# Optimization experiments

Hardware: AMD Instinct MI355X
Metric: run time of the kernel (lower is better)

## Reference

```python
import jax, jax.numpy as jnp
import numpy as np

# Model constants (from Equilibrium3BConfig + hardcoded MambaBlock args)
D_MODEL = 2560
D_INNER = 5120          # expand=2
N_STATE = 128           # d_state
HEADS = 80              # d_inner // headdim
P_HEAD = 64             # headdim
D_CONV = 4
CONV_DIM = D_INNER + 2 * N_STATE        # 5376 (x, B, C share the conv)
D_IN_PROJ = 2 * D_INNER + 2 * N_STATE + HEADS  # 10576 (z, xBC, dt)
N_EXPERTS = 16
TOP_K = 2
M_INTER = 864
MS_INTER = 1728
EPS = 1e-6


def _rms(x, w, eps=EPS):
    xf = x.astype(jnp.float32)
    xf = xf * jax.lax.rsqrt(jnp.mean(xf * xf, axis=-1, keepdims=True) + eps)
    return w * xf.astype(x.dtype)


def setup_inputs() -> dict:
    key = jax.random.key(0)
    ks = jax.random.split(key, 16)
    b, l = 1, 1024
    s = 0.02  # weight scale, keeps activations sane through the deep block
    return {
        "hidden_states": jax.random.normal(ks[0], (b, l, D_MODEL), jnp.float32),
        "w_in": jax.random.normal(ks[1], (D_MODEL, D_IN_PROJ), jnp.float32) * s,
        "conv_w": jax.random.normal(ks[2], (CONV_DIM, D_CONV), jnp.float32) * s,
        "conv_b": jnp.zeros((CONV_DIM,), jnp.float32),
        "dt_bias": jax.random.normal(ks[3], (HEADS,), jnp.float32) * s,
        "A_log": jax.random.normal(ks[4], (HEADS,), jnp.float32) * s,
        "D": jnp.ones((HEADS,), jnp.float32),
        "mamba_norm_w": jnp.ones((D_INNER,), jnp.float32),
        "w_out": jax.random.normal(ks[5], (D_INNER, D_MODEL), jnp.float32) * s,
        "ln1_w": jnp.ones((D_MODEL,), jnp.float32),
        "ln2_w": jnp.ones((D_MODEL,), jnp.float32),
        "router_w": jax.random.normal(ks[6], (D_MODEL, N_EXPERTS), jnp.float32) * s,
        "we_gate": jax.random.normal(ks[7], (N_EXPERTS, D_MODEL, M_INTER), jnp.float32) * s,
        "we_up": jax.random.normal(ks[8], (N_EXPERTS, D_MODEL, M_INTER), jnp.float32) * s,
        "we_down": jax.random.normal(ks[9], (N_EXPERTS, M_INTER, D_MODEL), jnp.float32) * s,
        "ws_gate": jax.random.normal(ks[10], (D_MODEL, MS_INTER), jnp.float32) * s,
        "ws_up": jax.random.normal(ks[11], (D_MODEL, MS_INTER), jnp.float32) * s,
        "ws_down": jax.random.normal(ks[12], (MS_INTER, D_MODEL), jnp.float32) * s,
    }


def _forward(hidden_states, w_in, conv_w, conv_b, dt_bias, A_log, D, mamba_norm_w,
             w_out, ln1_w, ln2_w, router_w, we_gate, we_up, we_down,
             ws_gate, ws_up, ws_down):
    b, l, d = hidden_states.shape

    # ---- Mamba2 (selective scan) sub-block ----
    residual = hidden_states
    x = _rms(hidden_states, ln1_w)
    zxbcdt = x @ w_in  # [b, l, 10576]
    z, xBC, dt = jnp.split(zxbcdt, [D_INNER, D_INNER + CONV_DIM], axis=-1)

    # depthwise causal conv over (x, B, C) channels, then SiLU
    xBC_t = xBC.transpose(0, 2, 1)  # [b, c, l]
    conv = jax.lax.conv_general_dilated(
        xBC_t, conv_w[:, None, :], (1,), [(D_CONV - 1, 0)],
        feature_group_count=CONV_DIM, dimension_numbers=("NCH", "OIH", "NCH"))
    xBC = jax.nn.silu((conv + conv_b[None, :, None]).transpose(0, 2, 1))
    xs, Bc, Cc = jnp.split(xBC, [D_INNER, D_INNER + N_STATE], axis=-1)

    dt = jax.nn.softplus(dt + dt_bias)          # [b, l, h]
    A = -jnp.exp(A_log)                          # [h]
    xh = xs.reshape(b, l, HEADS, P_HEAD)

    # time-major for scan
    dt_l = dt.transpose(1, 0, 2)                 # [l, b, h]
    xh_l = xh.transpose(1, 0, 2, 3)              # [l, b, h, p]
    B_l = Bc.transpose(1, 0, 2)                  # [l, b, n]
    C_l = Cc.transpose(1, 0, 2)                  # [l, b, n]

    def step(h, inp):
        dt_t, x_t, B_t, C_t = inp
        dA = jnp.exp(dt_t * A)                   # [b, h]
        h = h * dA[..., None, None] + (dt_t[..., None] * x_t)[..., None] * B_t[:, None, None, :]
        y = jnp.einsum("bhpn,bn->bhp", h, C_t)
        return h, y

    h0 = jnp.zeros((b, HEADS, P_HEAD, N_STATE), hidden_states.dtype)
    _, y_l = jax.lax.scan(step, h0, (dt_l, xh_l, B_l, C_l))
    y_l = y_l + D[None, None, :, None] * xh_l    # skip term
    y = y_l.transpose(1, 0, 2, 3).reshape(b, l, D_INNER)
    y = _rms(y * jax.nn.silu(z), mamba_norm_w)   # gated RMSNorm
    hidden = residual + y @ w_out

    # ---- DeepSeekMoE sub-block ----
    residual2 = hidden
    xm = _rms(hidden, ln2_w).reshape(b * l, d)
    logits = xm @ router_w
    probs = jax.nn.softmax(logits.astype(jnp.float32), axis=-1)
    topv, topi = jax.lax.top_k(probs, TOP_K)
    topv = topv / jnp.sum(topv, axis=-1, keepdims=True)  # renormalize top-k
    wdense = jnp.sum(jax.nn.one_hot(topi, N_EXPERTS, dtype=xm.dtype)
                     * topv[..., None].astype(xm.dtype), axis=1)  # [T, E]

    # routed experts (SwiGLU), dense-masked faithful math
    hexp = (jax.nn.silu(jnp.einsum("td,edm->tem", xm, we_gate))
            * jnp.einsum("td,edm->tem", xm, we_up))
    y_routed = jnp.einsum("tem,emd,te->td", hexp, we_down, wdense)

    # shared experts (single fused SwiGLU MLP)
    y_shared = (jax.nn.silu(xm @ ws_gate) * (xm @ ws_up)) @ ws_down

    moe = (y_routed + y_shared).reshape(b, l, d)
    return residual2 + moe


def reference(hidden_states, w_in, conv_w, conv_b, dt_bias, A_log, D, mamba_norm_w,
              w_out, ln1_w, ln2_w, router_w, we_gate, we_up, we_down,
              ws_gate, ws_up, ws_down):
    return _forward(hidden_states, w_in, conv_w, conv_b, dt_bias, A_log, D,
                    mamba_norm_w, w_out, ln1_w, ln2_w, router_w,
                    we_gate, we_up, we_down, ws_gate, ws_up, ws_down)
```

## Files before the change

### kernel.cpp

```cpp
#include <hip/hip_runtime.h>

typedef __attribute__((ext_vector_type(4))) float f32x4;
typedef __attribute__((ext_vector_type(8))) __bf16 bf16x8;
typedef __attribute__((ext_vector_type(4))) __bf16 bf16x4;
typedef __attribute__((ext_vector_type(8))) _Float16 f16x8;
typedef __attribute__((ext_vector_type(4))) _Float16 f16x4;

#define D_MODEL 2560
#define D_INNER 5120
#define N_STATE 128
#define HEADS 80
#define P_HEAD 64
#define CONV_DIM 5376
#define D_INPROJ 10576
#define SEQ 1024
#define NCHUNK 32
#define QCHUNK 32
#define NEXP 16
#define M_INTER 864
#define MS_INTER 1728
#define NSLOT 2048
#define NSLOTP 2176

__device__ __forceinline__ float siluf(float x) { return x / (1.f + __expf(-x)); }

__device__ __forceinline__ int swz_p(int k4, int P) {
  return (k4 & ~31) | ((((k4 >> 3) & 3) ^ P) << 3) | (k4 & 7);
}
__device__ __forceinline__ int swz64(int k4, int row) {
  return (k4 & ~63) | (((((k4 >> 3) & 7) ^ (row & 7)) << 3)) | (k4 & 7);
}

__device__ __forceinline__ void gl16(const __bf16* g, __bf16* l) {
  __builtin_amdgcn_global_load_lds((const __attribute__((address_space(1))) unsigned int*)g,
                                   (__attribute__((address_space(3))) unsigned int*)l, 16, 0, 0);
}

__device__ __forceinline__ float block_sum256(float v, float* red) {
#pragma unroll
  for (int m = 32; m > 0; m >>= 1) v += __shfl_xor(v, m, 64);
  int w = threadIdx.x >> 6;
  if ((threadIdx.x & 63) == 0) red[w] = v;
  __syncthreads();
  return red[0] + red[1] + red[2] + red[3];
}

template <bool FP16>
__global__ __launch_bounds__(256) void k_rmsnorm_p(const float* __restrict__ in,
                                                   const float* __restrict__ w,
                                                   float* __restrict__ f32out,
                                                   __bf16* __restrict__ ph,
                                                   __bf16* __restrict__ pdh,
                                                   __bf16* __restrict__ pdl, int D) {
  __shared__ float red[4];
  int t = blockIdx.x, tid = threadIdx.x;
  const float* x = in + (size_t)t * D;
  int nd4 = D >> 2;
  float ss = 0.f;
  for (int i = tid; i < nd4; i += 256) {
    float4 v = ((const float4*)x)[i];
    ss += v.x * v.x + v.y * v.y + v.z * v.z + v.w * v.w;
  }
  float tot = block_sum256(ss, red);
  float r = rsqrtf(tot / (float)D + 1e-6f);
  int P = (t >> 1) & 3;
  for (int i = tid; i < nd4; i += 256) {
    float4 v = ((const float4*)x)[i];
    float4 wv = ((const float4*)w)[i];
    float4 o;
    o.x = wv.x * v.x * r; o.y = wv.y * v.y * r; o.z = wv.z * v.z * r; o.w = wv.w * v.w * r;
    if (f32out) ((float4*)(f32out + (size_t)t * D))[i] = o;
    int p64 = swz64(i * 4, t);
    if constexpr (FP16) {
      f16x4 hv;
      hv[0] = (_Float16)o.x; hv[1] = (_Float16)o.y; hv[2] = (_Float16)o.z; hv[3] = (_Float16)o.w;
      *(f16x4*)&ph[(size_t)t * D + p64] = hv;
    } else {
      bf16x4 hv;
      hv[0] = (__bf16)o.x; hv[1] = (__bf16)o.y; hv[2] = (__bf16)o.z; hv[3] = (__bf16)o.w;
      *(bf16x4*)&ph[(size_t)t * D + p64] = hv;
    }
    if (pdh) {
      int p = swz_p(i * 4, P);
      bf16x4 hv, lv;
      hv[0] = (__bf16)o.x; hv[1] = (__bf16)o.y; hv[2] = (__bf16)o.z; hv[3] = (__bf16)o.w;
      lv[0] = (__bf16)(o.x - (float)hv[0]); lv[1] = (__bf16)(o.y - (float)hv[1]);
      lv[2] = (__bf16)(o.z - (float)hv[2]); lv[3] = (__bf16)(o.w - (float)hv[3]);
      *(bf16x4*)&pdh[(size_t)t * D + p] = hv;
      *(bf16x4*)&pdl[(size_t)t * D + p] = lv;
    }
  }
}

template <bool SPLIT, bool FP16>
__global__ __launch_bounds__(256) void k_transW(const float* __restrict__ W, int ld, int K, int N,
                                                __bf16* __restrict__ Th, __bf16* __restrict__ Tl) {
  __shared__ float T[64][65];
  const int n0 = blockIdx.x * 64, k0 = blockIdx.y * 64, tid = threadIdx.x;
#pragma unroll
  for (int i = 0; i < 16; i++) {
    int idx = tid + i * 256;
    int k = idx >> 6, n = idx & 63;
    float v = 0.f;
    if (n0 + n < N) v = W[(size_t)(k0 + k) * ld + n0 + n];
    T[k][n] = v;
  }
  __syncthreads();
#pragma unroll
  for (int i = 0; i < 4; i++) {
    int idx = tid + i * 256;
    int n = idx >> 4, p4 = (idx & 15) * 4;
    int nn = n0 + n;
    if constexpr (SPLIT) {
      int P = (nn >> 1) & 3;
      bf16x4 hv, lv;
#pragma unroll
      for (int e = 0; e < 4; e++) {
        int p = p4 + e;
        int kk = (p & ~31) | ((((p >> 3) & 3) ^ P) << 3) | (p & 7);
        float v = T[kk][n];
        __bf16 h = (__bf16)v;
        hv[e] = h;
        lv[e] = (__bf16)(v - (float)h);
      }
      *(bf16x4*)&Th[(size_t)nn * K + k0 + p4] = hv;
      *(bf16x4*)&Tl[(size_t)nn * K + k0 + p4] = lv;
    } else if constexpr (FP16) {
      f16x4 hv;
#pragma unroll
      for (int e = 0; e < 4; e++) {
        int p = p4 + e;
        int kk = swz64(p, nn);
        hv[e] = (_Float16)T[kk][n];
      }
      *(f16x4*)&Th[(size_t)nn * K + k0 + p4] = hv;
    } else {
      bf16x4 hv;
#pragma unroll
      for (int e = 0; e < 4; e++) {
        int p = p4 + e;
        int kk = swz64(p, nn);
        hv[e] = (__bf16)T[kk][n];
      }
      *(bf16x4*)&Th[(size_t)nn * K + k0 + p4] = hv;
    }
  }
}

template <bool SPLIT, bool FP16, int BK, bool PIPE>
__global__ __launch_bounds__(256) void k_gemm2(const __bf16* __restrict__ Ah,
                                               const __bf16* __restrict__ Al,
                                               const __bf16* __restrict__ Bh,
                                               const __bf16* __restrict__ Bl,
                                               float* __restrict__ C,
                                               int M, int N, int K, int ks, int nst) {
  constexpr int PLE = 128 * BK;
  constexpr int NPL = SPLIT ? 4 : 2;
  constexpr int NBUF = PIPE ? 2 : 1;
  constexpr int CALLS = PLE / 2048;
  constexpr int CPR = BK / 8;
  constexpr int RPC = 256 / CPR;
  constexpr int KSUB = BK / 32;
  __shared__ __bf16 lds[NBUF * NPL * PLE];

  const int tid = threadIdx.x;
  const int T = gridDim.x * gridDim.y * gridDim.z;
  const int linear = blockIdx.x + gridDim.x * (blockIdx.y + gridDim.y * blockIdx.z);
  const int s_idx = (linear & 7) * (T >> 3) + (linear >> 3);
  const int bm = s_idx & 7;
  const int g = s_idx >> 3;
  const int bn = g % gridDim.y;
  const int z = g / gridDim.y;

  const int m0 = bm * 128, n0 = bn * 128;
  const int s0 = (int)(((long long)z * nst) / ks);
  const int s1 = (int)(((long long)(z + 1) * nst) / ks);
  float* __restrict__ Cp = C + (size_t)z * M * N;

  const int lane = tid & 63, wid = tid >> 6;
  const int wr = wid >> 1, wc = wid & 1;
  const int l16 = lane & 15, kl = lane >> 4;

  const int srow = tid / CPR;
  const int schunk = (tid % CPR) * 8;
  size_t aB[CALLS], bB[CALLS];
#pragma unroll
  for (int i = 0; i < CALLS; i++) {
    aB[i] = (size_t)(m0 + srow + RPC * i) * K + schunk;
    bB[i] = (size_t)(n0 + srow + RPC * i) * K + schunk;
  }

  int aoff[4][KSUB], boff[4][KSUB];
#pragma unroll
  for (int mi = 0; mi < 4; mi++) {
    int ra = wr * 64 + mi * 16 + l16;
    int rb = wc * 64 + mi * 16 + l16;
#pragma unroll
    for (int kk = 0; kk < KSUB; kk++) {
      if constexpr (BK == 32) {
        aoff[mi][kk] = ra * 64 + ((kl ^ ((ra >> 1) & 3)) << 4);
        boff[mi][kk] = rb * 64 + ((kl ^ ((rb >> 1) & 3)) << 4);
      } else {
        aoff[mi][kk] = ra * (2 * BK) + (((kk * 4 + kl) ^ (ra & 7)) << 4);
        boff[mi][kk] = rb * (2 * BK) + (((kk * 4 + kl) ^ (rb & 7)) << 4);
      }
    }
  }

  f32x4 acc[4][4];
#pragma unroll
  for (int mi = 0; mi < 4; mi++)
#pragma unroll
    for (int ni = 0; ni < 4; ni++) acc[mi][ni] = f32x4{0.f, 0.f, 0.f, 0.f};

  auto STAGE = [&](int b, int kof) {
    __bf16* L = lds + (size_t)b * NPL * PLE;
#pragma unroll
    for (int i = 0; i < CALLS; i++) {
      gl16(Ah + aB[i] + kof, L + (tid + i * 256) * 8);
      gl16(Bh + bB[i] + kof, L + (SPLIT ? 2 : 1) * PLE + (tid + i * 256) * 8);
      if constexpr (SPLIT) {
        gl16(Al + aB[i] + kof, L + PLE + (tid + i * 256) * 8);
        gl16(Bl + bB[i] + kof, L + 3 * PLE + (tid + i * 256) * 8);
      }
    }
  };

  auto COMPUTE = [&](const __bf16* L) {
    const char* AsH = (const char*)L;
    const char* BsH = (const char*)(L + (SPLIT ? 2 : 1) * PLE);
#pragma unroll
    for (int kk = 0; kk < KSUB; kk++) {
      if constexpr (!SPLIT && FP16) {
        f16x8 ah[4], bh[4];
#pragma unroll
        for (int mi = 0; mi < 4; mi++) ah[mi] = *(const f16x8*)(AsH + aoff[mi][kk]);
#pragma unroll
        for (int ni = 0; ni < 4; ni++) bh[ni] = *(const f16x8*)(BsH + boff[ni][kk]);
#pragma unroll
        for (int mi = 0; mi < 4; mi++)
#pragma unroll
          for (int ni = 0; ni < 4; ni++)
            acc[mi][ni] = __builtin_amdgcn_mfma_f32_16x16x32_f16(ah[mi], bh[ni], acc[mi][ni], 0, 0, 0);
      } else {
        bf16x8 ah[4], bh[4];
#pragma unroll
        for (int mi = 0; mi < 4; mi++) ah[mi] = *(const bf16x8*)(AsH + aoff[mi][kk]);
#pragma unroll
        for (int ni = 0; ni < 4; ni++) bh[ni] = *(const bf16x8*)(BsH + boff[ni][kk]);
#pragma unroll
        for (int mi = 0; mi < 4; mi++)
#pragma unroll
          for (int ni = 0; ni < 4; ni++)
            acc[mi][ni] = __builtin_amdgcn_mfma_f32_16x16x32_bf16(ah[mi], bh[ni], acc[mi][ni], 0, 0, 0);
        if constexpr (SPLIT) {
          const char* AsL = (const char*)(L + PLE);
          const char* BsL = (const char*)(L + 3 * PLE);
          bf16x8 al[4], bl[4];
#pragma unroll
          for (int mi = 0; mi < 4; mi++) al[mi] = *(const bf16x8*)(AsL + aoff[mi][kk]);
#pragma unroll
          for (int ni = 0; ni < 4; ni++) bl[ni] = *(const bf16x8*)(BsL + boff[ni][kk]);
#pragma unroll
          for (int mi = 0; mi < 4; mi++)
#pragma unroll
            for (int ni = 0; ni < 4; ni++) {
              acc[mi][ni] = __builtin_amdgcn_mfma_f32_16x16x32_bf16(ah[mi], bl[ni], acc[mi][ni], 0, 0, 0);
              acc[mi][ni] = __builtin_amdgcn_mfma_f32_16x16x32_bf16(al[mi], bh[ni], acc[mi][ni], 0, 0, 0);
            }
        }
      }
    }
  };

  if constexpr (PIPE) {
    STAGE(0, s0 * BK);
    __syncthreads();
    int cur = 0;
    for (int s = s0; s < s1; ++s) {
      if (s + 1 < s1) STAGE(cur ^ 1, (s + 1) * BK);
      COMPUTE(lds + (size_t)cur * NPL * PLE);
      __syncthreads();
      cur ^= 1;
    }
  } else {
    for (int s = s0; s < s1; ++s) {
      __syncthreads();
      STAGE(0, s * BK);
      __syncthreads();
      COMPUTE(lds);
    }
  }

#pragma unroll
  for (int mi = 0; mi < 4; mi++)
#pragma unroll
    for (int ni = 0; ni < 4; ni++)
#pragma unroll
      for (int r = 0; r < 4; r++) {
        int row = m0 + wr * 64 + mi * 16 + kl * 4 + r;
        int col = n0 + wc * 64 + ni * 16 + l16;
        if (col < N) Cp[(size_t)row * N + col] = acc[mi][ni][r];
      }
}

template <bool RES>
__global__ void k_reduce(const float* __restrict__ Pp, int np, int n4,
                         const float* __restrict__ res, float* __restrict__ out) {
  int i = blockIdx.x * 256 + threadIdx.x;
  int stride = gridDim.x * 256;
  for (; i < n4; i += stride) {
    float4 a = ((const float4*)Pp)[i];
    for (int z = 1; z < np; z++) {
      float4 b = ((const float4*)Pp)[(size_t)z * n4 + i];
      a.x += b.x; a.y += b.y; a.z += b.z; a.w += b.w;
    }
    if constexpr (RES) {
      float4 r0 = ((const float4*)res)[i];
      a.x += r0.x; a.y += r0.y; a.z += r0.z; a.w += r0.w;
    }
    ((float4*)out)[i] = a;
  }
}

__global__ void k_dtfin(const float* __restrict__ dtP, const float* __restrict__ dt_bias,
                        const float* __restrict__ A_log, float* __restrict__ dtp,
                        float* __restrict__ dtA) {
  int t = blockIdx.x, h = threadIdx.x;
  if (h < HEADS) {
    float v = dt_bias[h];
#pragma unroll
    for (int z = 0; z < 8; z++) v += dtP[((size_t)z * SEQ + t) * 80 + h];
    float sp = fmaxf(v, 0.f) + log1pf(expf(-fabsf(v)));
    dtp[t * HEADS + h] = sp;
    dtA[t * HEADS + h] = sp * (-expf(A_log[h]));
  }
}

__global__ __launch_bounds__(256) void k_gatherA(const float* __restrict__ xm,
                                                 const int* __restrict__ perm,
                                                 __bf16* __restrict__ Aslots) {
  int s = blockIdx.x, tid = threadIdx.x;
  int t = perm[s];
  int P = (s >> 1) & 3;
  const float* src = xm + (size_t)t * D_MODEL;
  __bf16* dst = Aslots + (size_t)s * D_MODEL;
  for (int i = tid; i < D_MODEL / 4; i += 256) {
    float4 v = ((const float4*)src)[i];
    int p = swz_p(i * 4, P);
    bf16x4 h;
    h[0] = (__bf16)v.x; h[1] = (__bf16)v.y; h[2] = (__bf16)v.z; h[3] = (__bf16)v.w;
    *(bf16x4*)&dst[p] = h;
  }
}

template <int KS>
__global__ __launch_bounds__(256) void k_gemmE2(const __bf16* __restrict__ Aall,
                                                const float* __restrict__ Bg,
                                                float* __restrict__ Cp,
                                                const int* __restrict__ expOff,
                                                const int* __restrict__ expCnt,
                                                int N, int K, long long strideB) {
  __shared__ __bf16 Asl[2][128 * 32];
  __shared__ __bf16 Bsl[2][128][40];
  const int tid = threadIdx.x;
  const int bn = blockIdx.x, ks = blockIdx.y, e = blockIdx.z;
  const int cnt = expCnt[e], base = expOff[e];
  if (cnt == 0) return;
  const float* Bp = Bg + (long long)e * strideB;
  const int n0 = bn * 128;
  const int kChunk = K / KS, kBeg = ks * kChunk, nIter = kChunk / 32;
  float* __restrict__ Cpl = Cp + (size_t)ks * NSLOTP * N;
  const int lane = tid & 63, wid = tid >> 6;
  const int wr = wid >> 1, wc = wid & 1;
  const int l16 = lane & 15, kl = lane >> 4;
  const int kb = tid >> 5, cb = tid & 31;
  const int arow = tid >> 2, achk = (tid & 3) * 8;
  const bool bok = (n0 + cb * 4) < N;

  int boffs[4];
#pragma unroll
  for (int ni = 0; ni < 4; ni++) boffs[ni] = (wc * 64 + ni * 16 + l16) * 40 + kl * 8;

  for (int bm = 0; bm * 128 < cnt; ++bm) {
    const int rbase = base + bm * 128;
    int aoff[4];
#pragma unroll
    for (int mi = 0; mi < 4; mi++) {
      int r = wr * 64 + mi * 16 + l16;
      int P = ((rbase + r) >> 1) & 3;
      aoff[mi] = r * 64 + ((kl ^ P) << 4);
    }
    f32x4 acc[4][4];
#pragma unroll
    for (int mi = 0; mi < 4; mi++)
#pragma unroll
      for (int ni = 0; ni < 4; ni++) acc[mi][ni] = f32x4{0.f, 0.f, 0.f, 0.f};

    const size_t aBase = (size_t)(rbase + arow) * K + achk + kBeg;
    const size_t aBase2 = aBase + (size_t)64 * K;

    gl16(Aall + aBase, &Asl[0][tid * 8]);
    gl16(Aall + aBase2, &Asl[0][(tid + 256) * 8]);
    {
      const float* src = Bp + (size_t)(kBeg + kb * 4) * N + n0 + cb * 4;
      f32x4 bv[4];
#pragma unroll
      for (int j = 0; j < 4; j++)
        bv[j] = bok ? *(const f32x4*)(src + (size_t)j * N) : f32x4{0.f, 0.f, 0.f, 0.f};
#pragma unroll
      for (int e4 = 0; e4 < 4; e4++) {
        bf16x4 h;
        h[0] = (__bf16)bv[0][e4]; h[1] = (__bf16)bv[1][e4];
        h[2] = (__bf16)bv[2][e4]; h[3] = (__bf16)bv[3][e4];
        *(bf16x4*)&Bsl[0][cb * 4 + e4][kb * 4] = h;
      }
    }
    __syncthreads();
    int cur = 0;
    for (int kt = 0; kt < nIter; ++kt) {
      const bool more = (kt + 1 < nIter);
      f32x4 nv[4];
      if (more) {
        const int kOff = (kt + 1) * 32;
        gl16(Aall + aBase + kOff, &Asl[cur ^ 1][tid * 8]);
        gl16(Aall + aBase2 + kOff, &Asl[cur ^ 1][(tid + 256) * 8]);
        const float* src = Bp + (size_t)(kBeg + kOff + kb * 4) * N + n0 + cb * 4;
#pragma unroll
        for (int j = 0; j < 4; j++)
          nv[j] = bok ? *(const f32x4*)(src + (size_t)j * N) : f32x4{0.f, 0.f, 0.f, 0.f};
      }
      bf16x8 ah[4], bh[4];
#pragma unroll
      for (int mi = 0; mi < 4; mi++) ah[mi] = *(const bf16x8*)((const char*)&Asl[cur][0] + aoff[mi]);
#pragma unroll
      for (int ni = 0; ni < 4; ni++) bh[ni] = *(const bf16x8*)&Bsl[cur][0][boffs[ni]];
#pragma unroll
      for (int mi = 0; mi < 4; mi++)
#pragma unroll
        for (int ni = 0; ni < 4; ni++)
          acc[mi][ni] = __builtin_amdgcn_mfma_f32_16x16x32_bf16(ah[mi], bh[ni], acc[mi][ni], 0, 0, 0);
      if (more) {
#pragma unroll
        for (int e4 = 0; e4 < 4; e4++) {
          bf16x4 h;
          h[0] = (__bf16)nv[0][e4]; h[1] = (__bf16)nv[1][e4];
          h[2] = (__bf16)nv[2][e4]; h[3] = (__bf16)nv[3][e4];
          *(bf16x4*)&Bsl[cur ^ 1][cb * 4 + e4][kb * 4] = h;
        }
      }
      __syncthreads();
      cur ^= 1;
    }
#pragma unroll
    for (int mi = 0; mi < 4; mi++)
#pragma unroll
      for (int ni = 0; ni < 4; ni++)
#pragma unroll
        for (int r = 0; r < 4; r++) {
          int rl = bm * 128 + wr * 64 + mi * 16 + kl * 4 + r;
          int col = n0 + wc * 64 + ni * 16 + l16;
          if (rl < cnt && col < N) Cpl[(size_t)(base + rl) * N + col] = acc[mi][ni][r];
        }
  }
}

__global__ __launch_bounds__(256) void k_silumulE(const float* __restrict__ gP,
                                                  const float* __restrict__ uP,
                                                  const float* __restrict__ slotw,
                                                  __bf16* __restrict__ outp) {
  int s = blockIdx.x, tid = threadIdx.x;
  float w = slotw[s];
  int P = (s >> 1) & 3;
  const size_t PL = (size_t)NSLOTP * M_INTER;
  for (int i = tid; i < M_INTER / 4; i += 256) {
    f32x4 g = f32x4{0.f, 0.f, 0.f, 0.f}, u = f32x4{0.f, 0.f, 0.f, 0.f};
#pragma unroll
    for (int z = 0; z < 4; z++) {
      g += *(const f32x4*)&gP[z * PL + (size_t)s * M_INTER + i * 4];
      u += *(const f32x4*)&uP[z * PL + (size_t)s * M_INTER + i * 4];
    }
    int p = swz_p(i * 4, P);
    bf16x4 h;
    h[0] = (__bf16)(siluf(g[0]) * u[0] * w);
    h[1] = (__bf16)(siluf(g[1]) * u[1] * w);
    h[2] = (__bf16)(siluf(g[2]) * u[2] * w);
    h[3] = (__bf16)(siluf(g[3]) * u[3] * w);
    *(bf16x4*)&outp[(size_t)s * M_INTER + p] = h;
  }
}

__global__ __launch_bounds__(256) void k_silumul_sh2(const float* __restrict__ P4,
                                                     __bf16* __restrict__ outp) {
  int t = blockIdx.x, tid = threadIdx.x;
  const size_t PL = (size_t)SEQ * 3456;
  for (int i = tid; i < MS_INTER / 4; i += 256) {
    f32x4 g = f32x4{0.f, 0.f, 0.f, 0.f}, u = f32x4{0.f, 0.f, 0.f, 0.f};
#pragma unroll
    for (int z = 0; z < 4; z++) {
      g += *(const f32x4*)&P4[z * PL + (size_t)t * 3456 + i * 4];
      u += *(const f32x4*)&P4[z * PL + (size_t)t * 3456 + 1728 + i * 4];
    }
    int p = swz64(i * 4, t);
    bf16x4 h;
    h[0] = (__bf16)(siluf(g[0]) * u[0]);
    h[1] = (__bf16)(siluf(g[1]) * u[1]);
    h[2] = (__bf16)(siluf(g[2]) * u[2]);
    h[3] = (__bf16)(siluf(g[3]) * u[3]);
    *(bf16x4*)&outp[(size_t)t * MS_INTER + p] = h;
  }
}

__global__ void k_conv(const float* __restrict__ zx, const float* __restrict__ cw,
                       const float* __restrict__ cb, float* __restrict__ xBC) {
  int cidx = blockIdx.x * 256 + threadIdx.x;
  int t = blockIdx.y;
  if (cidx < CONV_DIM) {
    float acc = cb[cidx];
#pragma unroll
    for (int j = 0; j < 4; j++) {
      int tt = t - 3 + j;
      if (tt >= 0) acc += zx[(size_t)tt * D_INPROJ + D_INNER + cidx] * cw[cidx * 4 + j];
    }
    xBC[(size_t)t * CONV_DIM + cidx] = siluf(acc);
  }
}

__global__ __launch_bounds__(256) void k_scan_intra(
    const float* __restrict__ xBC, const float* __restrict__ dtp,
    const float* __restrict__ dtA, float* __restrict__ y, float* __restrict__ S,
    float* __restrict__ cumA, float* __restrict__ Atot) {
  __shared__ float Bs[32][128];
  __shared__ float Cs[32][128];
  __shared__ float Xs[32][68];
  __shared__ float Gs[32][33];
  __shared__ float da_s[32], a_s[32], dt_sh[32], w_sh[32];
  int c = blockIdx.x, h = blockIdx.y, tid = threadIdx.x;
  int t0 = c * QCHUNK;
#pragma unroll
  for (int i = 0; i < 4; i++) {
    int id = tid + 256 * i;
    int r = id >> 5, cc = id & 31;
    int sc = (cc ^ (r & 31)) * 4;
    *(float4*)&Bs[r][sc] = *(const float4*)&xBC[(size_t)(t0 + r) * CONV_DIM + D_INNER + cc * 4];
    *(float4*)&Cs[r][sc] = *(const float4*)&xBC[(size_t)(t0 + r) * CONV_DIM + D_INNER + N_STATE + cc * 4];
  }
#pragma unroll
  for (int i = 0; i < 2; i++) {
    int id = tid + 256 * i;
    int r = id >> 4, p4 = (id & 15) * 4;
    *(float4*)&Xs[r][p4] = *(const float4*)&xBC[(size_t)(t0 + r) * CONV_DIM + h * P_HEAD + p4];
  }
  if (tid < 32) {
    da_s[tid] = dtA[(size_t)(t0 + tid) * HEADS + h];
    dt_sh[tid] = dtp[(size_t)(t0 + tid) * HEADS + h];
  }
  __syncthreads();
  if (tid < 32) {
    float a = 0.f;
    for (int i = 0; i <= tid; i++) a += da_s[i];
    a_s[tid] = a;
    cumA[((size_t)c * HEADS + h) * QCHUNK + tid] = a;
  }
  __syncthreads();
  if (tid < 32) {
    w_sh[tid] = __expf(a_s[31] - a_s[tid]) * dt_sh[tid];
    if (tid == 0) Atot[c * HEADS + h] = a_s[31];
  }
  __syncthreads();
  {
    int tq = tid >> 4, sq = tid & 15;
    float gacc[2][2] = {{0.f, 0.f}, {0.f, 0.f}};
    for (int nc = 0; nc < 32; nc++) {
      float4 cv[2], bv[2];
#pragma unroll
      for (int j = 0; j < 2; j++) {
        int rt = tq * 2 + j;
        cv[j] = *(const float4*)&Cs[rt][(nc ^ (rt & 31)) * 4];
        int rs = sq * 2 + j;
        bv[j] = *(const float4*)&Bs[rs][(nc ^ (rs & 31)) * 4];
      }
#pragma unroll
      for (int j = 0; j < 2; j++)
#pragma unroll
        for (int jj = 0; jj < 2; jj++)
          gacc[j][jj] += cv[j].x * bv[jj].x + cv[j].y * bv[jj].y + cv[j].z * bv[jj].z + cv[j].w * bv[jj].w;
    }
#pragma unroll
    for (int j = 0; j < 2; j++)
#pragma unroll
      for (int jj = 0; jj < 2; jj++) {
        int t = tq * 2 + j, s = sq * 2 + jj;
        float arg = fminf(a_s[t] - a_s[s], 0.f);
        Gs[t][s] = (s <= t) ? gacc[j][jj] * __expf(arg) * dt_sh[s] : 0.f;
      }
  }
  __syncthreads();
  {
    int tq = tid >> 4, pq = tid & 15;
    float4 acc[2];
    acc[0] = float4{0.f, 0.f, 0.f, 0.f};
    acc[1] = float4{0.f, 0.f, 0.f, 0.f};
    for (int s = 0; s < 32; s++) {
      float4 xv = *(const float4*)&Xs[s][pq * 4];
#pragma unroll
      for (int j = 0; j < 2; j++) {
        float g0 = Gs[tq * 2 + j][s];
        acc[j].x += g0 * xv.x; acc[j].y += g0 * xv.y; acc[j].z += g0 * xv.z; acc[j].w += g0 * xv.w;
      }
    }
#pragma unroll
    for (int j = 0; j < 2; j++) {
      int t = tq * 2 + j;
      *(float4*)&y[(size_t)(t0 + t) * D_INNER + h * P_HEAD + pq * 4] = acc[j];
    }
  }
  {
    int p2 = tid >> 5, ncc = tid & 31;
    float4 acc[8];
#pragma unroll
    for (int j = 0; j < 8; j++) acc[j] = float4{0.f, 0.f, 0.f, 0.f};
    for (int s = 0; s < 32; s++) {
      float4 bvv = *(const float4*)&Bs[s][(ncc ^ (s & 31)) * 4];
#pragma unroll
      for (int j = 0; j < 8; j++) {
        float xw = Xs[s][p2 * 8 + j] * w_sh[s];
        acc[j].x += xw * bvv.x; acc[j].y += xw * bvv.y; acc[j].z += xw * bvv.z; acc[j].w += xw * bvv.w;
      }
    }
    size_t bb = ((size_t)(c * HEADS + h) * 64) * 128;
#pragma unroll
    for (int j = 0; j < 8; j++)
      *(float4*)&S[bb + (size_t)(p2 * 8 + j) * 128 + ncc * 4] = acc[j];
  }
}

__global__ void k_scan_state(float* __restrict__ S, const float* __restrict__ Atot) {
  int gid = blockIdx.x * 256 + threadIdx.x;
  int h = gid >> 13;
  int rem = gid & 8191;
  float run = 0.f;
#pragma unroll
  for (int c = 0; c < NCHUNK; c++) {
    size_t idx = ((size_t)(c * HEADS + h) << 13) + rem;
    float s = S[idx];
    S[idx] = run;
    run = run * __expf(Atot[c * HEADS + h]) + s;
  }
}

__global__ __launch_bounds__(256) void k_scan_inter(
    const float* __restrict__ xBC, const float* __restrict__ Hin,
    const float* __restrict__ cumA, const float* __restrict__ Dv,
    float* __restrict__ y) {
  __shared__ float Hs[64][128];
  __shared__ float Cs[32][128];
  __shared__ float a_l[32];
  int c = blockIdx.x, h = blockIdx.y, tid = threadIdx.x;
  int t0 = c * QCHUNK;
#pragma unroll
  for (int i = 0; i < 8; i++) {
    int id = tid + 256 * i;
    int r = id >> 5, cc = id & 31;
    *(float4*)&Hs[r][(cc ^ (r & 31)) * 4] =
        *(const float4*)&Hin[(((size_t)(c * HEADS + h) * 64 + r) << 7) + cc * 4];
  }
#pragma unroll
  for (int i = 0; i < 4; i++) {
    int id = tid + 256 * i;
    int r = id >> 5, cc = id & 31;
    *(float4*)&Cs[r][(cc ^ (r & 31)) * 4] =
        *(const float4*)&xBC[(size_t)(t0 + r) * CONV_DIM + D_INNER + N_STATE + cc * 4];
  }
  if (tid < 32) a_l[tid] = cumA[((size_t)c * HEADS + h) * QCHUNK + tid];
  __syncthreads();
  float Dh = Dv[h];
  int tq = tid >> 4, pq = tid & 15;
  float4 acc[2];
  acc[0] = float4{0.f, 0.f, 0.f, 0.f};
  acc[1] = float4{0.f, 0.f, 0.f, 0.f};
  for (int nc = 0; nc < 32; nc++) {
    float4 cv[2], hv[4];
#pragma unroll
    for (int j = 0; j < 2; j++) {
      int rt = tq * 2 + j;
      cv[j] = *(const float4*)&Cs[rt][(nc ^ (rt & 31)) * 4];
    }
#pragma unroll
    for (int jj = 0; jj < 4; jj++) {
      int rp = pq * 4 + jj;
      hv[jj] = *(const float4*)&Hs[rp][(nc ^ (rp & 31)) * 4];
    }
#pragma unroll
    for (int j = 0; j < 2; j++) {
      acc[j].x += cv[j].x * hv[0].x + cv[j].y * hv[0].y + cv[j].z * hv[0].z + cv[j].w * hv[0].w;
      acc[j].y += cv[j].x * hv[1].x + cv[j].y * hv[1].y + cv[j].z * hv[1].z + cv[j].w * hv[1].w;
      acc[j].z += cv[j].x * hv[2].x + cv[j].y * hv[2].y + cv[j].z * hv[2].z + cv[j].w * hv[2].w;
      acc[j].w += cv[j].x * hv[3].x + cv[j].y * hv[3].y + cv[j].z * hv[3].z + cv[j].w * hv[3].w;
    }
  }
#pragma unroll
  for (int j = 0; j < 2; j++) {
    int t = tq * 2 + j;
    float e = __expf(a_l[t]);
    float4 xv = *(const float4*)&xBC[(size_t)(t0 + t) * CONV_DIM + h * P_HEAD + pq * 4];
    size_t yoff = (size_t)(t0 + t) * D_INNER + h * P_HEAD + pq * 4;
    float4 yv = *(float4*)&y[yoff];
    yv.x += e * acc[j].x + Dh * xv.x;
    yv.y += e * acc[j].y + Dh * xv.y;
    yv.z += e * acc[j].z + Dh * xv.z;
    yv.w += e * acc[j].w + Dh * xv.w;
    *(float4*)&y[yoff] = yv;
  }
}

__global__ __launch_bounds__(256) void k_gatednorm_p(const float* __restrict__ y,
                                                     const float* __restrict__ zx,
                                                     const float* __restrict__ w,
                                                     __bf16* __restrict__ ph) {
  __shared__ float vbuf[D_INNER];
  __shared__ float red[4];
  int t = blockIdx.x, tid = threadIdx.x;
  float ss = 0.f;
  for (int i = tid; i < D_INNER / 4; i += 256) {
    float4 yv = *(const float4*)&y[(size_t)t * D_INNER + i * 4];
    float4 zv = *(const float4*)&zx[(size_t)t * D_INPROJ + i * 4];
    float4 v;
    v.x = yv.x * siluf(zv.x); v.y = yv.y * siluf(zv.y);
    v.z = yv.z * siluf(zv.z); v.w = yv.w * siluf(zv.w);
    *(float4*)&vbuf[i * 4] = v;
    ss += v.x * v.x + v.y * v.y + v.z * v.z + v.w * v.w;
  }
  float tot = block_sum256(ss, red);
  float r = rsqrtf(tot / (float)D_INNER + 1e-6f);
  for (int i = tid; i < D_INNER / 4; i += 256) {
    float4 v = *(const float4*)&vbuf[i * 4];
    float4 wv = *(const float4*)&w[i * 4];
    float4 o;
    o.x = wv.x * v.x * r; o.y = wv.y * v.y * r; o.z = wv.z * v.z * r; o.w = wv.w * v.w * r;
    int p = swz64(i * 4, t);
    f16x4 hv;
    hv[0] = (_Float16)o.x; hv[1] = (_Float16)o.y; hv[2] = (_Float16)o.z; hv[3] = (_Float16)o.w;
    *(f16x4*)&ph[(size_t)t * D_INNER + p] = hv;
  }
}

__global__ void k_zero(int* counts, int* cursor) {
  int i = threadIdx.x;
  if (i < NEXP) { counts[i] = 0; cursor[i] = 0; }
}

__global__ __launch_bounds__(256) void k_router(const float* __restrict__ xm,
                                                const float* __restrict__ Wr,
                                                int* __restrict__ top_i,
                                                float* __restrict__ top_v,
                                                int* __restrict__ counts) {
  __shared__ float part[16][17];
  __shared__ float lg[16];
  int t = blockIdx.x, tid = threadIdx.x;
  int e = tid & 15, seg = tid >> 4;
  const float* xr = xm + (size_t)t * D_MODEL;
  float s = 0.f;
  for (int i = 0; i < 160; i++) {
    int k = seg * 160 + i;
    s += xr[k] * Wr[(size_t)k * NEXP + e];
  }
  part[seg][e] = s;
  __syncthreads();
  if (tid < 16) {
    float l = 0.f;
    for (int g = 0; g < 16; g++) l += part[g][tid];
    lg[tid] = l;
  }
  __syncthreads();
  if (tid == 0) {
    float mx = lg[0];
    for (int i = 1; i < 16; i++) mx = fmaxf(mx, lg[i]);
    float pe[16];
    for (int i = 0; i < 16; i++) pe[i] = expf(lg[i] - mx);
    int i0 = 0; float v0 = pe[0];
    for (int i = 1; i < 16; i++) if (pe[i] > v0) { v0 = pe[i]; i0 = i; }
    int i1 = -1; float v1 = -1.f;
    for (int i = 0; i < 16; i++) if (i != i0 && pe[i] > v1) { v1 = pe[i]; i1 = i; }
    float inv = 1.f / (v0 + v1);
    top_i[t * 2] = i0; top_i[t * 2 + 1] = i1;
    top_v[t * 2] = v0 * inv; top_v[t * 2 + 1] = v1 * inv;
    atomicAdd(&counts[i0], 1);
    atomicAdd(&counts[i1], 1);
  }
}

__global__ void k_offsets(const int* counts, int* offs, int* cursor) {
  if (threadIdx.x == 0) {
    int s = 0;
    for (int e = 0; e < NEXP; e++) { offs[e] = s; cursor[e] = s; s += counts[e]; }
  }
}

__global__ void k_scatter(const int* __restrict__ top_i, const float* __restrict__ top_v,
                          int* __restrict__ cursor, int* __restrict__ perm,
                          int* __restrict__ slotOf, float* __restrict__ slotw) {
  int t = blockIdx.x * 256 + threadIdx.x;
  if (t < SEQ) {
    for (int k = 0; k < 2; k++) {
      int e = top_i[t * 2 + k];
      int pos = atomicAdd(&cursor[e], 1);
      perm[pos] = t;
      slotOf[t * 2 + k] = pos;
      slotw[pos] = top_v[t * 2 + k];
    }
  }
}

__global__ void k_final2(const float* __restrict__ hidden, const float* __restrict__ sh,
                         const float* __restrict__ dsP, const int* __restrict__ slotOf,
                         float* __restrict__ out) {
  int t = blockIdx.y;
  int d4 = (blockIdx.x * 256 + threadIdx.x) * 4;
  if (d4 < D_MODEL) {
    int s0 = slotOf[t * 2], s1 = slotOf[t * 2 + 1];
    f32x4 a = *(const f32x4*)&hidden[(size_t)t * D_MODEL + d4];
    f32x4 b = *(const f32x4*)&sh[(size_t)t * D_MODEL + d4];
    f32x4 acc = a + b;
    const size_t PL = (size_t)NSLOTP * D_MODEL;
#pragma unroll
    for (int z = 0; z < 3; z++) {
      acc += *(const f32x4*)&dsP[z * PL + (size_t)s0 * D_MODEL + d4];
      acc += *(const f32x4*)&dsP[z * PL + (size_t)s1 * D_MODEL + d4];
    }
    *(f32x4*)&out[(size_t)t * D_MODEL + d4] = acc;
  }
}

extern "C" void kernel_launch(void* const* d_in, const int* in_sizes, int n_in,
                              void* d_out, int out_size, void* d_ws, size_t ws_size,
                              hipStream_t stream) {
  const float* hs = (const float*)d_in[0];
  const float* w_in = (const float*)d_in[1];
  const float* conv_w = (const float*)d_in[2];
  const float* conv_b = (const float*)d_in[3];
  const float* dt_bias = (const float*)d_in[4];
  const float* A_log = (const float*)d_in[5];
  const float* Dv = (const float*)d_in[6];
  const float* mnw = (const float*)d_in[7];
  const float* w_out = (const float*)d_in[8];
  const float* ln1 = (const float*)d_in[9];
  const float* ln2 = (const float*)d_in[10];
  const float* router_w = (const float*)d_in[11];
  const float* we_gate = (const float*)d_in[12];
  const float* we_up = (const float*)d_in[13];
  const float* we_down = (const float*)d_in[14];
  const float* ws_gate = (const float*)d_in[15];
  const float* ws_up = (const float*)d_in[16];
  const float* ws_down = (const float*)d_in[17];

  char* base = (char*)d_ws;
  size_t off = 0;
  auto A = [&](size_t bytes) -> void* {
    void* p = base + off;
    off += (bytes + 255) & ~(size_t)255;
    return p;
  };
  float* xbc = (float*)A((size_t)SEQ * CONV_DIM * 4);
  float* xmf = (float*)A((size_t)SEQ * D_MODEL * 4);
  float* dtp = (float*)A((size_t)SEQ * HEADS * 4);
  float* dtA = (float*)A((size_t)SEQ * HEADS * 4);
  float* yf = (float*)A((size_t)SEQ * D_INNER * 4);
  float* cumA = (float*)A((size_t)NCHUNK * HEADS * QCHUNK * 4);
  float* Atot = (float*)A((size_t)NCHUNK * HEADS * 4);
  float* Sbuf = (float*)A((size_t)NCHUNK * HEADS * 64 * 128 * 4);
  float* hidden = (float*)A((size_t)SEQ * D_MODEL * 4);
  float* shout = (float*)A((size_t)SEQ * D_MODEL * 4);
  float* top_v = (float*)A(8192);
  float* slotw = (float*)A(8192);
  int* top_i = (int*)A(8192);
  int* counts = (int*)A(64);
  int* offs = (int*)A(64);
  int* cursor = (int*)A(64);
  int* perm = (int*)A(8192);
  int* slotOf = (int*)A(8192);
  __bf16* xp_h = (__bf16*)A((size_t)SEQ * D_MODEL * 2);
  __bf16* ybp_h = (__bf16*)A((size_t)SEQ * D_INNER * 2);
  __bf16* gbuf_bh = (__bf16*)A((size_t)SEQ * MS_INTER * 2);
  char* REG = (char*)A((size_t)163000000);

  __bf16* winT_h = (__bf16*)REG;
  float* zx = (float*)(REG + 60000000);
  float* partials = (float*)(REG + 104000000);
  __bf16* xdt_h = (__bf16*)(REG + 147000000);
  __bf16* xdt_l = (__bf16*)(REG + 152500000);
  __bf16* wdt_h = (__bf16*)(REG + 158000000);
  __bf16* wdt_l = (__bf16*)(REG + 158700000);
  float* dtP = (float*)(REG + 159400000);
  __bf16* woutT_h = (__bf16*)REG;
  __bf16* guT = (__bf16*)REG;
  __bf16* downT = (__bf16*)(REG + 18350080);
  float* partials4 = (float*)(REG + 30000000);
  __bf16* Aslots = (__bf16*)REG;
  __bf16* gsl = (__bf16*)(REG + 12000000);
  float* gateP = (float*)(REG + 16000000);
  float* upP = (float*)(REG + 47000000);
  float* dslotsP = (float*)(REG + 78000000);

  k_rmsnorm_p<true><<<SEQ, 256, 0, stream>>>(hs, ln1, nullptr, xp_h, xdt_h, xdt_l, D_MODEL);
  k_transW<false, true><<<dim3(166, 40), 256, 0, stream>>>(w_in, D_INPROJ, D_MODEL, D_INPROJ,
                                                           winT_h, nullptr);
  k_transW<true, false><<<dim3(2, 40), 256, 0, stream>>>(w_in + 10496, D_INPROJ, D_MODEL, 80,
                                                         wdt_h, wdt_l);
  k_gemm2<false, true, 64, true><<<dim3(8, 83, 1), 256, 0, stream>>>(
      xp_h, nullptr, winT_h, nullptr, zx, SEQ, D_INPROJ, D_MODEL, 1, 40);
  k_gemm2<true, false, 32, false><<<dim3(8, 1, 8), 256, 0, stream>>>(
      xdt_h, xdt_l, wdt_h, wdt_l, dtP, SEQ, 80, D_MODEL, 8, 80);
  k_dtfin<<<SEQ, 128, 0, stream>>>(dtP, dt_bias, A_log, dtp, dtA);
  k_conv<<<dim3(21, SEQ), 256, 0, stream>>>(zx, conv_w, conv_b, xbc);
  k_scan_intra<<<dim3(NCHUNK, HEADS), 256, 0, stream>>>(xbc, dtp, dtA, yf, Sbuf, cumA, Atot);
  k_scan_state<<<2560, 256, 0, stream>>>(Sbuf, Atot);
  k_scan_inter<<<dim3(NCHUNK, HEADS), 256, 0, stream>>>(xbc, Sbuf, cumA, Dv, yf);
  k_gatednorm_p<<<SEQ, 256, 0, stream>>>(yf, zx, mnw, ybp_h);
  k_transW<false, true><<<dim3(40, 80), 256, 0, stream>>>(w_out, D_MODEL, D_INNER, D_MODEL,
                                                          woutT_h, nullptr);
  k_gemm2<false, true, 64, true><<<dim3(8, 20, 4), 256, 0, stream>>>(
      ybp_h, nullptr, woutT_h, nullptr, partials, SEQ, D_MODEL, D_INNER, 4, 80);
  k_reduce<true><<<2048, 256, 0, stream>>>(partials, 4, SEQ * D_MODEL / 4, hs, hidden);

  k_rmsnorm_p<false><<<SEQ, 256, 0, stream>>>(hidden, ln2, xmf, xp_h, nullptr, nullptr, D_MODEL);
  k_zero<<<1, 64, 0, stream>>>(counts, cursor);
  k_router<<<SEQ, 256, 0, stream>>>(xmf, router_w, top_i, top_v, counts);
  k_offsets<<<1, 32, 0, stream>>>(counts, offs, cursor);
  k_scatter<<<4, 256, 0, stream>>>(top_i, top_v, cursor, perm, slotOf, slotw);

  k_transW<false, false><<<dim3(27, 40), 256, 0, stream>>>(ws_gate, MS_INTER, D_MODEL, MS_INTER,
                                                           guT, nullptr);
  k_transW<false, false><<<dim3(27, 40), 256, 0, stream>>>(ws_up, MS_INTER, D_MODEL, MS_INTER,
                                                           guT + (size_t)MS_INTER * D_MODEL, nullptr);
  k_gemm2<false, false, 64, true><<<dim3(8, 27, 4), 256, 0, stream>>>(
      xp_h, nullptr, guT, nullptr, partials4, SEQ, 3456, D_MODEL, 4, 40);
  k_silumul_sh2<<<SEQ, 256, 0, stream>>>(partials4, gbuf_bh);
  k_transW<false, false><<<dim3(40, 27), 256, 0, stream>>>(ws_down, D_MODEL, MS_INTER, D_MODEL,
                                                           downT, nullptr);
  k_gemm2<false, false, 64, true><<<dim3(8, 20, 4), 256, 0, stream>>>(
      gbuf_bh, nullptr, downT, nullptr, partials4, SEQ, D_MODEL, MS_INTER, 4, 27);
  k_reduce<false><<<2048, 256, 0, stream>>>(partials4, 4, SEQ * D_MODEL / 4, nullptr, shout);

  k_gatherA<<<NSLOT, 256, 0, stream>>>(xmf, perm, Aslots);
  k_gemmE2<4><<<dim3(7, 4, NEXP), 256, 0, stream>>>(Aslots, we_gate, gateP, offs, counts,
                                                    M_INTER, D_MODEL, (long long)D_MODEL * M_INTER);
  k_gemmE2<4><<<dim3(7, 4, NEXP), 256, 0, stream>>>(Aslots, we_up, upP, offs, counts,
                                                    M_INTER, D_MODEL, (long long)D_MODEL * M_INTER);
  k_silumulE<<<NSLOT, 256, 0, stream>>>(gateP, upP, slotw, gsl);
  k_gemmE2<3><<<dim3(20, 3, NEXP), 256, 0, stream>>>(gsl, we_down, dslotsP, offs, counts,
                                                     D_MODEL, M_INTER, (long long)M_INTER * D_MODEL);

  k_final2<<<dim3(3, SEQ), 256, 0, stream>>>(hidden, shout, dslotsP, slotOf, (float*)d_out);
}
```

Before: 877.6 us.

## Double SSM scan chunk length to 64 and store X in fp16 LDS

Changes the chunked SSD scan from 32 chunks of 32 tokens to 16 chunks of 64, rewriting the intra-chunk and inter-chunk kernels with 4x4 register tiles, a new XOR swizzle, and the G matrix stored in the C buffer's shared memory. Fewer chunks cut the size of the inter-chunk state tensor and the length of the sequential state recurrence, while each block does more intra-chunk work. X is held in fp16 in shared memory to fit within the LDS budget. This lowers the precision of the intra-chunk products and halves the number of blocks, which may reduce occupancy.

```diff
diff --git a/kernel.cpp b/kernel.cpp
--- a/kernel.cpp
+++ b/kernel.cpp
@@ -14,8 +14,8 @@
 #define CONV_DIM 5376
 #define D_INPROJ 10576
 #define SEQ 1024
-#define NCHUNK 32
-#define QCHUNK 32
+#define NCHUNK 16
+#define QCHUNK 64
 #define NEXP 16
 #define M_INTER 864
 #define MS_INTER 1728
@@ -530,88 +530,104 @@
     const float* __restrict__ xBC, const float* __restrict__ dtp,
     const float* __restrict__ dtA, float* __restrict__ y, float* __restrict__ S,
     float* __restrict__ cumA, float* __restrict__ Atot) {
-  __shared__ float Bs[32][128];
-  __shared__ float Cs[32][128];
-  __shared__ float Xs[32][68];
-  __shared__ float Gs[32][33];
-  __shared__ float da_s[32], a_s[32], dt_sh[32], w_sh[32];
+  __shared__ float Bs[64 * 128];
+  __shared__ float CG[64 * 128];
+  __shared__ _Float16 Xs[64 * 64];
+  __shared__ float da_s[64], a_s[64], dt_sh[64], w_sh[64];
   int c = blockIdx.x, h = blockIdx.y, tid = threadIdx.x;
   int t0 = c * QCHUNK;
 #pragma unroll
+  for (int i = 0; i < 8; i++) {
+    int id = tid + 256 * i;
+    int r = id >> 5, nc = id & 31;
+    int sc = (nc ^ ((r >> 2) & 7)) * 4;
+    *(float4*)&Bs[r * 128 + sc] = *(const float4*)&xBC[(size_t)(t0 + r) * CONV_DIM + D_INNER + nc * 4];
+    *(float4*)&CG[r * 128 + sc] = *(const float4*)&xBC[(size_t)(t0 + r) * CONV_DIM + D_INNER + N_STATE + nc * 4];
+  }
+#pragma unroll
   for (int i = 0; i < 4; i++) {
     int id = tid + 256 * i;
-    int r = id >> 5, cc = id & 31;
-    int sc = (cc ^ (r & 31)) * 4;
-    *(float4*)&Bs[r][sc] = *(const float4*)&xBC[(size_t)(t0 + r) * CONV_DIM + D_INNER + cc * 4];
-    *(float4*)&Cs[r][sc] = *(const float4*)&xBC[(size_t)(t0 + r) * CONV_DIM + D_INNER + N_STATE + cc * 4];
-  }
-#pragma unroll
-  for (int i = 0; i < 2; i++) {
-    int id = tid + 256 * i;
     int r = id >> 4, p4 = (id & 15) * 4;
-    *(float4*)&Xs[r][p4] = *(const float4*)&xBC[(size_t)(t0 + r) * CONV_DIM + h * P_HEAD + p4];
-  }
-  if (tid < 32) {
+    float4 v = *(const float4*)&xBC[(size_t)(t0 + r) * CONV_DIM + h * P_HEAD + p4];
+    f16x4 hv;
+    hv[0] = (_Float16)v.x; hv[1] = (_Float16)v.y; hv[2] = (_Float16)v.z; hv[3] = (_Float16)v.w;
+    *(f16x4*)&Xs[r * 64 + p4] = hv;
+  }
+  if (tid < 64) {
     da_s[tid] = dtA[(size_t)(t0 + tid) * HEADS + h];
     dt_sh[tid] = dtp[(size_t)(t0 + tid) * HEADS + h];
   }
   __syncthreads();
-  if (tid < 32) {
+  if (tid < 64) {
     float a = 0.f;
     for (int i = 0; i <= tid; i++) a += da_s[i];
     a_s[tid] = a;
     cumA[((size_t)c * HEADS + h) * QCHUNK + tid] = a;
   }
   __syncthreads();
-  if (tid < 32) {
-    w_sh[tid] = __expf(a_s[31] - a_s[tid]) * dt_sh[tid];
-    if (tid == 0) Atot[c * HEADS + h] = a_s[31];
+  if (tid < 64) {
+    w_sh[tid] = __expf(a_s[63] - a_s[tid]) * dt_sh[tid];
+    if (tid == 0) Atot[c * HEADS + h] = a_s[63];
+  }
+  __syncthreads();
+  float gacc[4][4];
+  {
+    int tq = tid >> 4, sq = tid & 15;
+#pragma unroll
+    for (int j = 0; j < 4; j++)
+#pragma unroll
+      for (int jj = 0; jj < 4; jj++) gacc[j][jj] = 0.f;
+    for (int nc = 0; nc < 32; nc++) {
+      float4 cv[4], bv[4];
+#pragma unroll
+      for (int j = 0; j < 4; j++) {
+        int rt = tq * 4 + j;
+        cv[j] = *(const float4*)&CG[rt * 128 + ((nc ^ ((rt >> 2) & 7)) * 4)];
+        int rs = sq * 4 + j;
+        bv[j] = *(const float4*)&Bs[rs * 128 + ((nc ^ ((rs >> 2) & 7)) * 4)];
+      }
+#pragma unroll
+      for (int j = 0; j < 4; j++)
+#pragma unroll
+        for (int jj = 0; jj < 4; jj++)
+          gacc[j][jj] += cv[j].x * bv[jj].x + cv[j].y * bv[jj].y + cv[j].z * bv[jj].z + cv[j].w * bv[jj].w;
+    }
   }
   __syncthreads();
   {
     int tq = tid >> 4, sq = tid & 15;
-    float gacc[2][2] = {{0.f, 0.f}, {0.f, 0.f}};
-    for (int nc = 0; nc < 32; nc++) {
-      float4 cv[2], bv[2];
-#pragma unroll
-      for (int j = 0; j < 2; j++) {
-        int rt = tq * 2 + j;
-        cv[j] = *(const float4*)&Cs[rt][(nc ^ (rt & 31)) * 4];
-        int rs = sq * 2 + j;
-        bv[j] = *(const float4*)&Bs[rs][(nc ^ (rs & 31)) * 4];
-      }
-#pragma unroll
-      for (int j = 0; j < 2; j++)
-#pragma unroll
-        for (int jj = 0; jj < 2; jj++)
-          gacc[j][jj] += cv[j].x * bv[jj].x + cv[j].y * bv[jj].y + cv[j].z * bv[jj].z + cv[j].w * bv[jj].w;
-    }
-#pragma unroll
-    for (int j = 0; j < 2; j++)
-#pragma unroll
-      for (int jj = 0; jj < 2; jj++) {
-        int t = tq * 2 + j, s = sq * 2 + jj;
+#pragma unroll
+    for (int j = 0; j < 4; j++) {
+      int t = tq * 4 + j;
+      f32x4 gr;
+#pragma unroll
+      for (int jj = 0; jj < 4; jj++) {
+        int s = sq * 4 + jj;
         float arg = fminf(a_s[t] - a_s[s], 0.f);
-        Gs[t][s] = (s <= t) ? gacc[j][jj] * __expf(arg) * dt_sh[s] : 0.f;
-      }
+        gr[jj] = (s <= t) ? gacc[j][jj] * __expf(arg) * dt_sh[s] : 0.f;
+      }
+      *(f32x4*)&CG[t * 64 + ((sq ^ (t & 7)) * 4)] = gr;
+    }
   }
   __syncthreads();
   {
     int tq = tid >> 4, pq = tid & 15;
-    float4 acc[2];
-    acc[0] = float4{0.f, 0.f, 0.f, 0.f};
-    acc[1] = float4{0.f, 0.f, 0.f, 0.f};
-    for (int s = 0; s < 32; s++) {
-      float4 xv = *(const float4*)&Xs[s][pq * 4];
-#pragma unroll
-      for (int j = 0; j < 2; j++) {
-        float g0 = Gs[tq * 2 + j][s];
-        acc[j].x += g0 * xv.x; acc[j].y += g0 * xv.y; acc[j].z += g0 * xv.z; acc[j].w += g0 * xv.w;
-      }
-    }
-#pragma unroll
-    for (int j = 0; j < 2; j++) {
-      int t = tq * 2 + j;
+    float4 acc[4];
+#pragma unroll
+    for (int j = 0; j < 4; j++) acc[j] = float4{0.f, 0.f, 0.f, 0.f};
+    for (int s = 0; s < 64; s++) {
+      f16x4 xh = *(const f16x4*)&Xs[s * 64 + pq * 4];
+      float xv0 = (float)xh[0], xv1 = (float)xh[1], xv2 = (float)xh[2], xv3 = (float)xh[3];
+#pragma unroll
+      for (int j = 0; j < 4; j++) {
+        int t = tq * 4 + j;
+        float g = CG[t * 64 + (((s >> 2) ^ (t & 7)) * 4) + (s & 3)];
+        acc[j].x += g * xv0; acc[j].y += g * xv1; acc[j].z += g * xv2; acc[j].w += g * xv3;
+      }
+    }
+#pragma unroll
+    for (int j = 0; j < 4; j++) {
+      int t = tq * 4 + j;
       *(float4*)&y[(size_t)(t0 + t) * D_INNER + h * P_HEAD + pq * 4] = acc[j];
     }
   }
@@ -620,11 +636,12 @@
     float4 acc[8];
 #pragma unroll
     for (int j = 0; j < 8; j++) acc[j] = float4{0.f, 0.f, 0.f, 0.f};
-    for (int s = 0; s < 32; s++) {
-      float4 bvv = *(const float4*)&Bs[s][(ncc ^ (s & 31)) * 4];
+    for (int s = 0; s < 64; s++) {
+      float4 bvv = *(const float4*)&Bs[s * 128 + ((ncc ^ ((s >> 2) & 7)) * 4)];
+      float ws = w_sh[s];
 #pragma unroll
       for (int j = 0; j < 8; j++) {
-        float xw = Xs[s][p2 * 8 + j] * w_sh[s];
+        float xw = (float)Xs[s * 64 + p2 * 8 + j] * ws;
         acc[j].x += xw * bvv.x; acc[j].y += xw * bvv.y; acc[j].z += xw * bvv.z; acc[j].w += xw * bvv.w;
       }
     }
@@ -653,46 +670,37 @@
     const float* __restrict__ xBC, const float* __restrict__ Hin,
     const float* __restrict__ cumA, const float* __restrict__ Dv,
     float* __restrict__ y) {
-  __shared__ float Hs[64][128];
-  __shared__ float Cs[32][128];
-  __shared__ float a_l[32];
+  __shared__ float Hs[64 * 128];
+  __shared__ float Cs[64 * 128];
+  __shared__ float a_l[64];
   int c = blockIdx.x, h = blockIdx.y, tid = threadIdx.x;
   int t0 = c * QCHUNK;
 #pragma unroll
   for (int i = 0; i < 8; i++) {
     int id = tid + 256 * i;
-    int r = id >> 5, cc = id & 31;
-    *(float4*)&Hs[r][(cc ^ (r & 31)) * 4] =
-        *(const float4*)&Hin[(((size_t)(c * HEADS + h) * 64 + r) << 7) + cc * 4];
-  }
-#pragma unroll
-  for (int i = 0; i < 4; i++) {
-    int id = tid + 256 * i;
-    int r = id >> 5, cc = id & 31;
-    *(float4*)&Cs[r][(cc ^ (r & 31)) * 4] =
-        *(const float4*)&xBC[(size_t)(t0 + r) * CONV_DIM + D_INNER + N_STATE + cc * 4];
-  }
-  if (tid < 32) a_l[tid] = cumA[((size_t)c * HEADS + h) * QCHUNK + tid];
+    int r = id >> 5, nc = id & 31;
+    int sc = (nc ^ ((r >> 2) & 7)) * 4;
+    *(float4*)&Hs[r * 128 + sc] = *(const float4*)&Hin[(((size_t)(c * HEADS + h) * 64 + r) << 7) + nc * 4];
+    *(float4*)&Cs[r * 128 + sc] = *(const float4*)&xBC[(size_t)(t0 + r) * CONV_DIM + D_INNER + N_STATE + nc * 4];
+  }
+  if (tid < 64) a_l[tid] = cumA[((size_t)c * HEADS + h) * QCHUNK + tid];
   __syncthreads();
   float Dh = Dv[h];
   int tq = tid >> 4, pq = tid & 15;
-  float4 acc[2];
-  acc[0] = float4{0.f, 0.f, 0.f, 0.f};
-  acc[1] = float4{0.f, 0.f, 0.f, 0.f};
+  float4 acc[4];
+#pragma unroll
+  for (int j = 0; j < 4; j++) acc[j] = float4{0.f, 0.f, 0.f, 0.f};
   for (int nc = 0; nc < 32; nc++) {
-    float4 cv[2], hv[4];
-#pragma unroll
-    for (int j = 0; j < 2; j++) {
-      int rt = tq * 2 + j;
-      cv[j] = *(const float4*)&Cs[rt][(nc ^ (rt & 31)) * 4];
-    }
-#pragma unroll
-    for (int jj = 0; jj < 4; jj++) {
-      int rp = pq * 4 + jj;
-      hv[jj] = *(const float4*)&Hs[rp][(nc ^ (rp & 31)) * 4];
-    }
-#pragma unroll
-    for (int j = 0; j < 2; j++) {
+    float4 cv[4], hv[4];
+#pragma unroll
+    for (int j = 0; j < 4; j++) {
+      int rt = tq * 4 + j;
+      cv[j] = *(const float4*)&Cs[rt * 128 + ((nc ^ ((rt >> 2) & 7)) * 4)];
+      int rp = pq * 4 + j;
+      hv[j] = *(const float4*)&Hs[rp * 128 + ((nc ^ ((rp >> 2) & 7)) * 4)];
+    }
+#pragma unroll
+    for (int j = 0; j < 4; j++) {
       acc[j].x += cv[j].x * hv[0].x + cv[j].y * hv[0].y + cv[j].z * hv[0].z + cv[j].w * hv[0].w;
       acc[j].y += cv[j].x * hv[1].x + cv[j].y * hv[1].y + cv[j].z * hv[1].z + cv[j].w * hv[1].w;
       acc[j].z += cv[j].x * hv[2].x + cv[j].y * hv[2].y + cv[j].z * hv[2].z + cv[j].w * hv[2].w;
@@ -700,8 +708,8 @@
     }
   }
 #pragma unroll
-  for (int j = 0; j < 2; j++) {
-    int t = tq * 2 + j;
+  for (int j = 0; j < 4; j++) {
+    int t = tq * 4 + j;
     float e = __expf(a_l[t]);
     float4 xv = *(const float4*)&xBC[(size_t)(t0 + t) * CONV_DIM + h * P_HEAD + pq * 4];
     size_t yoff = (size_t)(t0 + t) * D_INNER + h * P_HEAD + pq * 4;
```

After: 791.0 us. -9.9%, faster.
